# Performance work log

Hardware: AMD Instinct MI355X
Metric: run time of the kernel (lower is better)

Reference implementation:

```python
import jax, jax.numpy as jnp
import numpy as np

# Hard-coded model hyperparams (RuntimeParams)
B, L, H, NH, FF, DEPTH = 256, 256, 128, 8, 512, 4
PEAK, NCAT, CVOC, KMAX, NNUM, NDIM, TSLOT = 500000, 8, 50001, 8, 4, 32, 256
SCALE = (H // NH) ** -0.5


def _ln(x, g, b):
    m = x.mean(-1, keepdims=True)
    v = ((x - m) ** 2).mean(-1, keepdims=True)
    return (x - m) / jnp.sqrt(v + 1e-5) * g + b


def _block(x, mask, p):
    ln1_g, ln1_b, qw, qb, ow, ob, w1, b1, w2, b2, ln2_g, ln2_b = p
    b, n, c = x.shape
    src = _ln(x, ln1_g, ln1_b)
    qkv = (src @ qw + qb).reshape(b, n, 3, NH, c // NH).transpose(2, 0, 3, 1, 4)
    q, k, v = qkv[0], qkv[1], qkv[2]  # [b, nh, n, dh]
    dots = jnp.einsum('bhid,bhjd->bhij', q, k) * SCALE
    dots = jnp.where(mask[:, None, None, :], dots, -jnp.inf)
    attn = jax.nn.softmax(dots, axis=-1)
    out = jnp.einsum('bhij,bhjd->bhid', attn, v).transpose(0, 2, 1, 3).reshape(b, n, c)
    x = x + out @ ow + ob
    h = _ln(x, ln2_g, ln2_b)
    h = jax.nn.gelu(h @ w1 + b1, approximate=False) @ w2 + b2
    return x + h


def _encode(cat_vals, cat_lens, num_arr, cat_tables, num_W):
    # Vectorized form of the per-sample _encode_fields python loop:
    # per categorical field: mean of embeddings over the ragged value list
    # per numeric field: bias-free linear projection; then mean over all fields.
    emb = cat_tables[jnp.arange(NCAT)[None, :, None], cat_vals]  # [B,F,K,H]
    pos = (jnp.arange(KMAX)[None, None, :] < cat_lens[:, :, None]).astype(emb.dtype)
    fc = (emb * pos[..., None]).sum(2) / cat_lens[:, :, None].astype(emb.dtype)  # [B,F,H]
    fn = jnp.einsum('bfd,fdh->bfh', num_arr, num_W)  # [B,Fn,H]
    return (fc.sum(1) + fn.sum(1)) / (NCAT + NNUM)  # mean over all fields


def setup_inputs() -> dict:
    key = jax.random.key(0)
    ks = iter(jax.random.split(key, 40))
    nk = lambda: next(ks)
    d = {}
    d['item_seq'] = jax.random.randint(nk(), (B, L), 0, PEAK + 5)
    d['action_seq'] = jax.random.randint(nk(), (B, L), 0, 5)
    d['time_diff'] = jax.random.randint(nk(), (B, L), 0, TSLOT)
    seq_lens = jax.random.randint(nk(), (B,), L // 2, L + 1)
    d['mask'] = jnp.arange(L)[None, :] < seq_lens[:, None]
    for pre in ('u', 'i'):
        vals = jax.random.randint(nk(), (B, NCAT, KMAX), 1, CVOC)
        lens = jax.random.randint(nk(), (B, NCAT), 1, KMAX + 1)
        vals = jnp.where(jnp.arange(KMAX)[None, None, :] < lens[:, :, None], vals, 0)
        d[pre + '_cat_vals'] = vals
        d[pre + '_cat_lens'] = lens
        d[pre + '_num'] = jax.random.normal(nk(), (B, NNUM, NDIM), dtype=jnp.float32)
    s = 0.02
    d['item_table'] = (jax.random.normal(nk(), (PEAK + 5, H), dtype=jnp.float32) * s).at[0].set(0.0)
    d['act_table'] = jax.random.normal(nk(), (5, H), dtype=jnp.float32) * s
    d['time_table'] = jax.random.normal(nk(), (TSLOT, H), dtype=jnp.float32) * s
    d['cat_tables'] = (jax.random.normal(nk(), (NCAT, CVOC, H), dtype=jnp.float32) * s).at[:, 0, :].set(0.0)
    d['num_W'] = jax.random.normal(nk(), (NNUM, NDIM, H), dtype=jnp.float32) * s
    d['global_token'] = jax.random.normal(nk(), (1, 1, H), dtype=jnp.float32)
    d['ln1_g'] = jnp.ones((DEPTH, H)); d['ln1_b'] = jnp.zeros((DEPTH, H))
    d['qkv_w'] = jax.random.normal(nk(), (DEPTH, H, 3 * H), dtype=jnp.float32) * s
    d['qkv_b'] = jnp.zeros((DEPTH, 3 * H))
    d['out_w'] = jax.random.normal(nk(), (DEPTH, H, H), dtype=jnp.float32) * s
    d['out_b'] = jnp.zeros((DEPTH, H))
    d['mlp_w1'] = jax.random.normal(nk(), (DEPTH, H, FF), dtype=jnp.float32) * s
    d['mlp_b1'] = jnp.zeros((DEPTH, FF))
    d['mlp_w2'] = jax.random.normal(nk(), (DEPTH, FF, H), dtype=jnp.float32) * s
    d['mlp_b2'] = jnp.zeros((DEPTH, H))
    d['ln2_g'] = jnp.ones((DEPTH, H)); d['ln2_b'] = jnp.zeros((DEPTH, H))
    d['bott_w'] = jax.random.normal(nk(), (H, H), dtype=jnp.float32) * s
    d['bott_b'] = jnp.zeros((H,))
    d['cls_w'] = jax.random.normal(nk(), (H, 1), dtype=jnp.float32) * s
    d['cls_b'] = jnp.zeros((1,))
    return d


def reference(item_seq, action_seq, time_diff, mask, u_cat_vals, u_cat_lens, u_num,
              i_cat_vals, i_cat_lens, i_num, item_table, act_table, time_table,
              cat_tables, num_W, global_token, ln1_g, ln1_b, qkv_w, qkv_b,
              out_w, out_b, mlp_w1, mlp_b1, mlp_w2, mlp_b2, ln2_g, ln2_b,
              bott_w, bott_b, cls_w, cls_b):
    b = item_seq.shape[0]
    seq_feat = item_table[item_seq] + act_table[action_seq] + time_table[time_diff]  # [B,L,H]
    u = _encode(u_cat_vals, u_cat_lens, u_num, cat_tables, num_W)[:, None, :]
    i = _encode(i_cat_vals, i_cat_lens, i_num, cat_tables, num_W)[:, None, :]
    cls = jnp.broadcast_to(global_token, (b, 1, H))
    x = jnp.concatenate([cls, u, i, seq_feat], axis=1)  # [B, 3+L, H]
    fmask = jnp.concatenate([jnp.ones((b, 3), dtype=bool), mask], axis=1)
    for dd in range(DEPTH):
        p = (ln1_g[dd], ln1_b[dd], qkv_w[dd], qkv_b[dd], out_w[dd], out_b[dd],
             mlp_w1[dd], mlp_b1[dd], mlp_w2[dd], mlp_b2[dd], ln2_g[dd], ln2_b[dd])
        x = _block(x, fmask, p)
    latent = x[:, 0, :]
    logits = (jax.nn.relu(latent @ bott_w + bott_b) @ cls_w + cls_b)[:, 0]
    embed = latent / jnp.maximum(jnp.linalg.norm(latent, axis=-1, keepdims=True), 1e-12)
    return logits, embed
```

## Files before the change

### kernel.cpp

```cpp
#include <hip/hip_runtime.h>
#include <cstdio>

#define BATCH 256
#define SEQL 256
#define NPOS 259
#define TTOK (BATCH*NPOS)
#define HD 128
#define NHEAD 8
#define FF 512
#define DEPTH 4
#define CVOC 50001

typedef unsigned short u16;
typedef unsigned int u32;
typedef __bf16 bf16x8 __attribute__((ext_vector_type(8)));
typedef float f32x4 __attribute__((ext_vector_type(4)));
typedef float f32x16 __attribute__((ext_vector_type(16)));

typedef const __attribute__((address_space(1))) u32 gas_u32;
typedef __attribute__((address_space(3))) u32 las_u32;
#define GLOAD16(gptr, lptr) \
  __builtin_amdgcn_global_load_lds((gas_u32*)(gptr), (las_u32*)(lptr), 16, 0, 0)

#define QSCALE 0.36067376022224085f

__device__ __forceinline__ u16 f2bf(float f) {
  u32 i = __float_as_uint(f);
  u32 r = (i + 0x7FFFu + ((i >> 16) & 1u)) >> 16;
  return (u16)r;
}

__global__ void k_transpose_all(const float* __restrict__ qkv_w, const float* __restrict__ out_w,
                                const float* __restrict__ w1, const float* __restrict__ w2,
                                u16* __restrict__ wT) {
  int idx = blockIdx.x * 256 + threadIdx.x;
  const float* in; int K, N, local;
  if (idx < 196608)      { in = qkv_w; K = 128; N = 384; local = idx; }
  else if (idx < 262144) { in = out_w; K = 128; N = 128; local = idx - 196608; }
  else if (idx < 524288) { in = w1;    K = 128; N = 512; local = idx - 262144; }
  else if (idx < 786432) { in = w2;    K = 512; N = 128; local = idx - 524288; }
  else return;
  int k = local % K; int rem = local / K; int n = rem % N; int d = rem / N;
  wT[idx] = f2bf(in[(d * K + k) * N + n]);
}

__global__ __launch_bounds__(128)
void k_build(const int* __restrict__ item_seq, const int* __restrict__ act_seq,
             const int* __restrict__ tdiff,
             const int* __restrict__ ucv, const int* __restrict__ ucl, const float* __restrict__ unum,
             const int* __restrict__ icv, const int* __restrict__ icl, const float* __restrict__ inum,
             const float* __restrict__ item_t, const float* __restrict__ act_t,
             const float* __restrict__ time_t, const float* __restrict__ cat_t,
             const float* __restrict__ numW, const float* __restrict__ gtok,
             const float* __restrict__ g, const float* __restrict__ be,
             float* __restrict__ x, u16* __restrict__ src) {
  int pos = blockIdx.x, b = blockIdx.y, h = threadIdx.x;
  float v;
  if (pos == 0) {
    v = gtok[h];
  } else if (pos <= 2) {
    const int* cv = (pos == 1) ? ucv : icv;
    const int* cl = (pos == 1) ? ucl : icl;
    const float* nm = (pos == 1) ? unum : inum;
    float acc = 0.f;
    for (int f = 0; f < 8; ++f) {
      float s = 0.f;
      for (int k = 0; k < 8; ++k) {
        int idx = cv[(b * 8 + f) * 8 + k];
        s += cat_t[((size_t)f * CVOC + idx) * HD + h];
      }
      acc += s / (float)cl[b * 8 + f];
    }
    for (int f = 0; f < 4; ++f)
      for (int d = 0; d < 32; ++d)
        acc += nm[(b * 4 + f) * 32 + d] * numW[(f * 32 + d) * HD + h];
    v = acc * (1.f / 12.f);
  } else {
    int l = pos - 3;
    v = item_t[(size_t)item_seq[b * SEQL + l] * HD + h]
      + act_t[(size_t)act_seq[b * SEQL + l] * HD + h]
      + time_t[(size_t)tdiff[b * SEQL + l] * HD + h];
  }
  size_t t = (size_t)b * NPOS + pos;
  x[t * HD + h] = v;
  __shared__ float red[2][2];
  float s = v, s2 = v * v;
  #pragma unroll
  for (int o = 32; o; o >>= 1) { s += __shfl_xor(s, o); s2 += __shfl_xor(s2, o); }
  if ((h & 63) == 0) { red[h >> 6][0] = s; red[h >> 6][1] = s2; }
  __syncthreads();
  float S = red[0][0] + red[1][0], S2 = red[0][1] + red[1][1];
  float mean = S * (1.f / HD);
  float rstd = rsqrtf(S2 * (1.f / HD) - mean * mean + 1e-5f);
  src[t * HD + h] = f2bf((v - mean) * rstd * g[h] + be[h]);
}

template <int NCH, int ACT, bool QS>
__global__ __launch_bounds__(256)
void k_gemm_nres(const u16* __restrict__ X, const u16* __restrict__ WT,
                 const float* __restrict__ bias, u16* __restrict__ outp) {
  const int K = 128, N = NCH * 128;
  __shared__ __align__(16) u16 lA[4][128 * 32];
  __shared__ __align__(16) u16 lB[128 * 32];
  const int tid = threadIdx.x;
  const int wave = tid >> 6, lane = tid & 63;
  const int row0 = blockIdx.x * 128;
  const int wr = (wave >> 1) * 64, wc = (wave & 1) * 64;
  const int sr = lane >> 2;
  const int sc = ((lane & 3) ^ ((lane >> 3) & 3)) << 3;
  const int q = lane & 15;
  const int cg = lane >> 4;
  const int rdoff = ((cg ^ ((q >> 1) & 3)) << 3);
  #pragma unroll
  for (int s = 0; s < 8; ++s) {
    int kt = s & 3, rg = 2 * wave + (s >> 2);
    int r = rg * 16 + sr;
    GLOAD16(X + (size_t)(row0 + r) * K + kt * 32 + sc, &lA[kt][rg * 512]);
  }
  const u16* gB0 = WT + (size_t)(wave * 16 + sr) * K + sc;
  const u16* gB1 = WT + (size_t)(64 + wave * 16 + sr) * K + sc;
  u16* lB0 = &lB[wave * 512];
  u16* lB1 = &lB[2048 + wave * 512];
  for (int nc = 0; nc < NCH; ++nc) {
    const size_t nbase = (size_t)nc * 128 * K;
    f32x4 acc[4][4] = {};
    for (int k0 = 0; k0 < K; k0 += 32) {
      __syncthreads();
      GLOAD16(gB0 + nbase + k0, lB0);
      GLOAD16(gB1 + nbase + k0, lB1);
      __syncthreads();
      const int kt = k0 >> 5;
      bf16x8 af[4], bf[4];
      #pragma unroll
      for (int i = 0; i < 4; ++i)
        af[i] = *(const bf16x8*)&lA[kt][(wr + i * 16 + q) * 32 + rdoff];
      #pragma unroll
      for (int j = 0; j < 4; ++j)
        bf[j] = *(const bf16x8*)&lB[(wc + j * 16 + q) * 32 + rdoff];
      #pragma unroll
      for (int i = 0; i < 4; ++i)
        #pragma unroll
        for (int j = 0; j < 4; ++j)
          acc[i][j] = __builtin_amdgcn_mfma_f32_16x16x32_bf16(af[i], bf[j], acc[i][j], 0, 0, 0);
    }
    const int rg4 = cg * 4;
    const float scl = (QS && nc == 0) ? QSCALE : 1.f;
    #pragma unroll
    for (int i = 0; i < 4; ++i) {
      #pragma unroll
      for (int j = 0; j < 4; ++j) {
        int col = nc * 128 + wc + j * 16 + q;
        float bv = bias[col];
        #pragma unroll
        for (int jj = 0; jj < 4; ++jj) {
          int row = row0 + wr + i * 16 + rg4 + jj;
          float v = acc[i][j][jj] + bv;
          if (ACT == 1) v = 0.5f * v * (1.f + erff(v * 0.70710678118654752f));
          if (QS) v *= scl;
          outp[(size_t)row * N + col] = f2bf(v);
        }
      }
    }
  }
}

__global__ __launch_bounds__(256)
void k_gemm_ln(const u16* __restrict__ X, const u16* __restrict__ WT,
               const float* __restrict__ bias, float* __restrict__ xio,
               const float* __restrict__ g, const float* __restrict__ be,
               u16* __restrict__ srcout, int K) {
  __shared__ __align__(16) u16 lA[128 * 32];
  __shared__ __align__(16) u16 lB[128 * 32];
  __shared__ float part[128][2][2];
  const int tid = threadIdx.x;
  const int wave = tid >> 6, lane = tid & 63;
  const int row0 = blockIdx.x * 128;
  const int wr = (wave >> 1) * 64, wc = (wave & 1) * 64;
  const int whalf = wave & 1;
  const int sr = lane >> 2;
  const int sc = ((lane & 3) ^ ((lane >> 3) & 3)) << 3;
  const u16* gA0 = X  + (size_t)(row0 + wave * 16 + sr) * K + sc;
  const u16* gA1 = X  + (size_t)(row0 + 64 + wave * 16 + sr) * K + sc;
  const u16* gB0 = WT + (size_t)(wave * 16 + sr) * K + sc;
  const u16* gB1 = WT + (size_t)(64 + wave * 16 + sr) * K + sc;
  u16* lA0 = &lA[wave * 512];
  u16* lA1 = &lA[2048 + wave * 512];
  u16* lB0 = &lB[wave * 512];
  u16* lB1 = &lB[2048 + wave * 512];
  const int q = lane & 15;
  const int cg = lane >> 4;
  const int rdoff = ((cg ^ ((q >> 1) & 3)) << 3);
  f32x4 acc[4][4] = {};
  for (int k0 = 0; k0 < K; k0 += 32) {
    __syncthreads();
    GLOAD16(gA0 + k0, lA0);
    GLOAD16(gA1 + k0, lA1);
    GLOAD16(gB0 + k0, lB0);
    GLOAD16(gB1 + k0, lB1);
    __syncthreads();
    bf16x8 af[4], bf[4];
    #pragma unroll
    for (int i = 0; i < 4; ++i)
      af[i] = *(const bf16x8*)&lA[(wr + i * 16 + q) * 32 + rdoff];
    #pragma unroll
    for (int j = 0; j < 4; ++j)
      bf[j] = *(const bf16x8*)&lB[(wc + j * 16 + q) * 32 + rdoff];
    #pragma unroll
    for (int i = 0; i < 4; ++i)
      #pragma unroll
      for (int j = 0; j < 4; ++j)
        acc[i][j] = __builtin_amdgcn_mfma_f32_16x16x32_bf16(af[i], bf[j], acc[i][j], 0, 0, 0);
  }
  const int rg4 = cg * 4;
  float ps[4][4], ps2[4][4];
  #pragma unroll
  for (int i = 0; i < 4; ++i)
    #pragma unroll
    for (int jj = 0; jj < 4; ++jj) { ps[i][jj] = 0.f; ps2[i][jj] = 0.f; }
  #pragma unroll
  for (int i = 0; i < 4; ++i) {
    #pragma unroll
    for (int j = 0; j < 4; ++j) {
      int col = wc + j * 16 + q;
      float bv = bias[col];
      #pragma unroll
      for (int jj = 0; jj < 4; ++jj) {
        int row = row0 + wr + i * 16 + rg4 + jj;
        float xv = xio[(size_t)row * 128 + col] + acc[i][j][jj] + bv;
        acc[i][j][jj] = xv;
        ps[i][jj] += xv;
        ps2[i][jj] += xv * xv;
      }
    }
  }
  #pragma unroll
  for (int o = 1; o < 16; o <<= 1) {
    #pragma unroll
    for (int i = 0; i < 4; ++i)
      #pragma unroll
      for (int jj = 0; jj < 4; ++jj) {
        ps[i][jj]  += __shfl_xor(ps[i][jj], o);
        ps2[i][jj] += __shfl_xor(ps2[i][jj], o);
      }
  }
  if (q == 0) {
    #pragma unroll
    for (int i = 0; i < 4; ++i)
      #pragma unroll
      for (int jj = 0; jj < 4; ++jj) {
        int rl = wr + i * 16 + rg4 + jj;
        part[rl][whalf][0] = ps[i][jj];
        part[rl][whalf][1] = ps2[i][jj];
      }
  }
  __syncthreads();
  #pragma unroll
  for (int i = 0; i < 4; ++i) {
    #pragma unroll
    for (int jj = 0; jj < 4; ++jj) {
      int rl = wr + i * 16 + rg4 + jj;
      float S  = part[rl][0][0] + part[rl][1][0];
      float S2 = part[rl][0][1] + part[rl][1][1];
      float mean = S * (1.f / 128.f);
      float rstd = rsqrtf(S2 * (1.f / 128.f) - mean * mean + 1e-5f);
      int row = row0 + rl;
      #pragma unroll
      for (int j = 0; j < 4; ++j) {
        int col = wc + j * 16 + q;
        float xv = acc[i][j][jj];
        xio[(size_t)row * 128 + col] = xv;
        srcout[(size_t)row * 128 + col] = f2bf((xv - mean) * rstd * g[col] + be[col]);
      }
    }
  }
}

#define VSTR2 296
__global__ __launch_bounds__(576)
void k_attn(const u16* __restrict__ qkv, const int* __restrict__ mask,
            u16* __restrict__ out) {
  int h = blockIdx.x, b = blockIdx.y;
  __shared__ __align__(16) u16 Klin[9 * 512];
  __shared__ __align__(16) u16 Vt[16 * VSTR2];
  __shared__ int part[4];
  const int tid = threadIdx.x;
  if (tid < 256) {
    int mv = (mask[b * SEQL + tid] != 0) ? 1 : 0;
    #pragma unroll
    for (int o = 32; o; o >>= 1) mv += __shfl_xor(mv, o);
    if ((tid & 63) == 0) part[tid >> 6] = mv;
  }
  {
    int r = tid >> 1, h2 = tid & 1;
    uint4 val = make_uint4(0, 0, 0, 0);
    if (r < NPOS)
      val = *(const uint4*)&qkv[((size_t)(b * NPOS + r)) * 384 + h * 16 + 128 + h2 * 8];
    *(uint4*)&Klin[(r >> 5) * 512 + h2 * 256 + (r & 31) * 8] = val;
  }
  if (tid < 288) {
    int r = tid;
    u16 tmp[16];
    if (r < NPOS) {
      const u16* vp = &qkv[((size_t)(b * NPOS + r)) * 384 + h * 16 + 256];
      *(uint4*)&tmp[0] = *(const uint4*)&vp[0];
      *(uint4*)&tmp[8] = *(const uint4*)&vp[8];
    } else {
      #pragma unroll
      for (int d = 0; d < 16; ++d) tmp[d] = 0;
    }
    #pragma unroll
    for (int d = 0; d < 16; ++d) Vt[d * VSTR2 + r] = tmp[d];
  }
  __syncthreads();
  const int nvalid = part[0] + part[1] + part[2] + part[3] + 3;
  const int ktiles = (nvalid + 31) >> 5;
  const int wave = tid >> 6, lane = tid & 63;
  const int q5 = lane & 31, hi = lane >> 5;
  const f32x16 zf = {};
  const int qt = wave;
  int qrow = qt * 32 + q5;
  int qr = (qrow < NPOS) ? qrow : (NPOS - 1);
  bf16x8 qf = *(const bf16x8*)&qkv[((size_t)(b * NPOS + qr)) * 384 + h * 16 + hi * 8];
  float m = -1e30f, l = 0.f;
  f32x16 acc = {};
  for (int kt = 0; kt < ktiles; ++kt) {
    bf16x8 kf = *(const bf16x8*)&Klin[kt * 512 + lane * 8];
    __builtin_amdgcn_s_setprio(1);
    f32x16 s4 = __builtin_amdgcn_mfma_f32_32x32x16_bf16(kf, qf, zf, 0, 0, 0);
    __builtin_amdgcn_s_setprio(0);
    float p[16];
    float tmax = -1e30f;
    #pragma unroll
    for (int r = 0; r < 16; ++r) {
      int kr = kt * 32 + (r & 3) + 8 * (r >> 2) + 4 * hi;
      float v = (kr < nvalid) ? s4[r] : -1e30f;
      p[r] = v;
      tmax = fmaxf(tmax, v);
    }
    tmax = fmaxf(tmax, __shfl_xor(tmax, 32));
    float mnew = fmaxf(m, tmax);
    float fac = exp2f(m - mnew);
    float tsum = 0.f;
    #pragma unroll
    for (int r = 0; r < 16; ++r) { p[r] = exp2f(p[r] - mnew); tsum += p[r]; }
    tsum += __shfl_xor(tsum, 32);
    l = l * fac + tsum;
    m = mnew;
    #pragma unroll
    for (int r = 0; r < 8; ++r) acc[r] *= fac;
    u32 w[8], xw[8];
    #pragma unroll
    for (int i = 0; i < 8; ++i)
      asm("v_cvt_pk_bf16_f32 %0, %1, %2" : "=v"(w[i]) : "v"(p[2 * i]), "v"(p[2 * i + 1]));
    #pragma unroll
    for (int i = 0; i < 8; ++i) xw[i] = (u32)__shfl_xor((int)w[i], 32);
    union { u32 u[4]; bf16x8 v; } f1, f2;
    if (hi) {
      f1.u[0] = xw[2]; f1.u[1] = xw[3]; f1.u[2] = w[2]; f1.u[3] = w[3];
      f2.u[0] = xw[6]; f2.u[1] = xw[7]; f2.u[2] = w[6]; f2.u[3] = w[7];
    } else {
      f1.u[0] = w[0]; f1.u[1] = w[1]; f1.u[2] = xw[0]; f1.u[3] = xw[1];
      f2.u[0] = w[4]; f2.u[1] = w[5]; f2.u[2] = xw[4]; f2.u[3] = xw[5];
    }
    bf16x8 vf0 = {}, vf1 = {};
    if (q5 < 16) {
      vf0 = *(const bf16x8*)&Vt[q5 * VSTR2 + kt * 32 + hi * 8];
      vf1 = *(const bf16x8*)&Vt[q5 * VSTR2 + kt * 32 + 16 + hi * 8];
    }
    __builtin_amdgcn_s_setprio(1);
    acc = __builtin_amdgcn_mfma_f32_32x32x16_bf16(vf0, f1.v, acc, 0, 0, 0);
    acc = __builtin_amdgcn_mfma_f32_32x32x16_bf16(vf1, f2.v, acc, 0, 0, 0);
    __builtin_amdgcn_s_setprio(0);
  }
  if (qrow < NPOS) {
    float linv = 1.f / l;
    u16* op = &out[((size_t)(b * NPOS + qrow)) * HD + h * 16];
    u32 w0 = (u32)f2bf(acc[0] * linv) | ((u32)f2bf(acc[1] * linv) << 16);
    u32 w1 = (u32)f2bf(acc[2] * linv) | ((u32)f2bf(acc[3] * linv) << 16);
    u32 w2 = (u32)f2bf(acc[4] * linv) | ((u32)f2bf(acc[5] * linv) << 16);
    u32 w3 = (u32)f2bf(acc[6] * linv) | ((u32)f2bf(acc[7] * linv) << 16);
    *(uint2*)&op[4 * hi] = make_uint2(w0, w1);
    *(uint2*)&op[8 + 4 * hi] = make_uint2(w2, w3);
  }
}

__global__ __launch_bounds__(128)
void k_head(const float* __restrict__ x, const float* __restrict__ bw,
            const float* __restrict__ bb, const float* __restrict__ cw,
            const float* __restrict__ cb, float* __restrict__ dout) {
  int b = blockIdx.x, n = threadIdx.x;
  __shared__ float lat[HD];
  __shared__ float redp[2], redss[2];
  float lv = x[((size_t)b * NPOS) * HD + n];
  lat[n] = lv;
  __syncthreads();
  float t = 0.f;
  for (int k = 0; k < HD; ++k) t += lat[k] * bw[k * HD + n];
  t += bb[n];
  t = fmaxf(t, 0.f);
  float p = t * cw[n];
  float ss = lv * lv;
  #pragma unroll
  for (int o = 32; o; o >>= 1) { p += __shfl_xor(p, o); ss += __shfl_xor(ss, o); }
  if ((n & 63) == 0) { redp[n >> 6] = p; redss[n >> 6] = ss; }
  __syncthreads();
  float psum = redp[0] + redp[1];
  float ssum = redss[0] + redss[1];
  if (n == 0) dout[b] = psum + cb[0];
  float nrm = fmaxf(sqrtf(ssum), 1e-12f);
  dout[256 + (size_t)b * HD + n] = lv / nrm;
}

extern "C" void kernel_launch(void* const* d_in, const int* in_sizes, int n_in,
                              void* d_out, int out_size, void* d_ws, size_t ws_size,
                              hipStream_t stream) {
  const int* item_seq = (const int*)d_in[0];
  const int* action_seq = (const int*)d_in[1];
  const int* time_diff = (const int*)d_in[2];
  const int* mask = (const int*)d_in[3];
  const int* u_cv = (const int*)d_in[4];
  const int* u_cl = (const int*)d_in[5];
  const float* u_num = (const float*)d_in[6];
  const int* i_cv = (const int*)d_in[7];
  const int* i_cl = (const int*)d_in[8];
  const float* i_num = (const float*)d_in[9];
  const float* item_t = (const float*)d_in[10];
  const float* act_t = (const float*)d_in[11];
  const float* time_t = (const float*)d_in[12];
  const float* cat_t = (const float*)d_in[13];
  const float* num_W = (const float*)d_in[14];
  const float* gtok = (const float*)d_in[15];
  const float* ln1_g = (const float*)d_in[16];
  const float* ln1_b = (const float*)d_in[17];
  const float* qkv_w = (const float*)d_in[18];
  const float* qkv_b = (const float*)d_in[19];
  const float* out_w = (const float*)d_in[20];
  const float* out_b = (const float*)d_in[21];
  const float* w1 = (const float*)d_in[22];
  const float* b1 = (const float*)d_in[23];
  const float* w2 = (const float*)d_in[24];
  const float* b2 = (const float*)d_in[25];
  const float* ln2_g = (const float*)d_in[26];
  const float* ln2_b = (const float*)d_in[27];
  const float* bott_w = (const float*)d_in[28];
  const float* bott_b = (const float*)d_in[29];
  const float* cls_w = (const float*)d_in[30];
  const float* cls_b = (const float*)d_in[31];

  const size_t off_x   = 0;
  const size_t off_src = 33947648;
  const size_t off_big = 50921472;
  const size_t off_wT  = 118816768;
  const size_t need    = 120389632;
  if (ws_size < need) {
    fprintf(stderr, "kernel_launch: ws_size %zu < needed %zu\n", ws_size, need);
    return;
  }
  char* ws = (char*)d_ws;
  float* x   = (float*)(ws + off_x);
  u16* src   = (u16*)(ws + off_src);
  u16* big   = (u16*)(ws + off_big);
  u16* wT    = (u16*)(ws + off_wT);
  u16* qkvT  = wT;
  u16* outT  = wT + 196608;
  u16* w1T   = wT + 262144;
  u16* w2T   = wT + 524288;

  k_transpose_all<<<3072, 256, 0, stream>>>(qkv_w, out_w, w1, w2, wT);

  k_build<<<dim3(NPOS, BATCH), 128, 0, stream>>>(
      item_seq, action_seq, time_diff, u_cv, u_cl, u_num, i_cv, i_cl, i_num,
      item_t, act_t, time_t, cat_t, num_W, gtok, ln1_g, ln1_b, x, src);

  const int rt = TTOK / 128;
  for (int dd = 0; dd < DEPTH; ++dd) {
    k_gemm_nres<3, 0, true><<<rt, 256, 0, stream>>>(
        src, qkvT + dd * 49152, qkv_b + dd * 384, big);
    k_attn<<<dim3(NHEAD, BATCH), 576, 0, stream>>>(big, mask, src);
    k_gemm_ln<<<dim3(rt, 1), 256, 0, stream>>>(
        src, outT + dd * 16384, out_b + dd * HD, x,
        ln2_g + dd * HD, ln2_b + dd * HD, src, 128);
    k_gemm_nres<4, 1, false><<<rt, 256, 0, stream>>>(
        src, w1T + dd * 65536, b1 + dd * FF, big);
    const float* ng = (dd < 3) ? (ln1_g + (dd + 1) * HD) : (ln1_g + dd * HD);
    const float* nb = (dd < 3) ? (ln1_b + (dd + 1) * HD) : (ln1_b + dd * HD);
    k_gemm_ln<<<dim3(rt, 1), 256, 0, stream>>>(
        big, w2T + dd * 65536, b2 + dd * HD, x, ng, nb, src, 512);
  }

  k_head<<<BATCH, 128, 0, stream>>>(x, bott_w, bott_b, cls_w, cls_b, (float*)d_out);
}
```

Measured before the change: 784.8 us.

## Fuse residual-LayerNorm GEMMs with following QKV and MLP-up GEMMs via LDS-resident activations

Merges each residual+LayerNorm GEMM with the GEMM that consumes its output. The normalized 128-wide tile is written into shared memory in the swizzled layout and reused directly as the A operand for the next GEMM: MLP up-projection with GELU, or the next layer's QKV projection with Q scaling. This removes the bf16 round-trip of the LN output through global memory and two kernel launches per layer. In exchange each block does more serial work, uses more shared memory, and the workspace grows to hold separate QKV and hidden buffers. The last layer uses a plain residual GEMM instead.

```diff
diff --git a/kernel.cpp b/kernel.cpp
--- a/kernel.cpp
+++ b/kernel.cpp
@@ -164,19 +164,176 @@
   }
 }
 
+template <int K1, int NCH2, int ACT2, bool QS2>
 __global__ __launch_bounds__(256)
-void k_gemm_ln(const u16* __restrict__ X, const u16* __restrict__ WT,
-               const float* __restrict__ bias, float* __restrict__ xio,
-               const float* __restrict__ g, const float* __restrict__ be,
-               u16* __restrict__ srcout, int K) {
-  __shared__ __align__(16) u16 lA[128 * 32];
-  __shared__ __align__(16) u16 lB[128 * 32];
+void k_fused(const u16* __restrict__ X, const u16* __restrict__ WT1,
+             const float* __restrict__ bias1, float* __restrict__ xio,
+             const float* __restrict__ g, const float* __restrict__ be,
+             const u16* __restrict__ WT2, const float* __restrict__ bias2,
+             u16* __restrict__ out2) {
+  __shared__ __align__(16) u16 sA[4][128 * 32];
+  __shared__ __align__(16) u16 sB[128 * 32];
   __shared__ float part[128][2][2];
   const int tid = threadIdx.x;
   const int wave = tid >> 6, lane = tid & 63;
   const int row0 = blockIdx.x * 128;
   const int wr = (wave >> 1) * 64, wc = (wave & 1) * 64;
   const int whalf = wave & 1;
+  const int sr = lane >> 2;
+  const int sc = ((lane & 3) ^ ((lane >> 3) & 3)) << 3;
+  const int q = lane & 15;
+  const int cg = lane >> 4;
+  const int rdoff = ((cg ^ ((q >> 1) & 3)) << 3);
+  const int rg4 = cg * 4;
+  {
+    const u16* gA0 = X + (size_t)(row0 + wave * 16 + sr) * K1 + sc;
+    const u16* gA1 = X + (size_t)(row0 + 64 + wave * 16 + sr) * K1 + sc;
+    const u16* gB0 = WT1 + (size_t)(wave * 16 + sr) * K1 + sc;
+    const u16* gB1 = WT1 + (size_t)(64 + wave * 16 + sr) * K1 + sc;
+    u16* lA0 = &sA[0][wave * 512];
+    u16* lA1 = &sA[0][2048 + wave * 512];
+    u16* lB0 = &sB[wave * 512];
+    u16* lB1 = &sB[2048 + wave * 512];
+    f32x4 acc[4][4] = {};
+    for (int k0 = 0; k0 < K1; k0 += 32) {
+      __syncthreads();
+      GLOAD16(gA0 + k0, lA0);
+      GLOAD16(gA1 + k0, lA1);
+      GLOAD16(gB0 + k0, lB0);
+      GLOAD16(gB1 + k0, lB1);
+      __syncthreads();
+      bf16x8 af[4], bf[4];
+      #pragma unroll
+      for (int i = 0; i < 4; ++i)
+        af[i] = *(const bf16x8*)&sA[0][(wr + i * 16 + q) * 32 + rdoff];
+      #pragma unroll
+      for (int j = 0; j < 4; ++j)
+        bf[j] = *(const bf16x8*)&sB[(wc + j * 16 + q) * 32 + rdoff];
+      #pragma unroll
+      for (int i = 0; i < 4; ++i)
+        #pragma unroll
+        for (int j = 0; j < 4; ++j)
+          acc[i][j] = __builtin_amdgcn_mfma_f32_16x16x32_bf16(af[i], bf[j], acc[i][j], 0, 0, 0);
+    }
+    float ps[4][4], ps2[4][4];
+    #pragma unroll
+    for (int i = 0; i < 4; ++i)
+      #pragma unroll
+      for (int jj = 0; jj < 4; ++jj) { ps[i][jj] = 0.f; ps2[i][jj] = 0.f; }
+    #pragma unroll
+    for (int i = 0; i < 4; ++i) {
+      #pragma unroll
+      for (int j = 0; j < 4; ++j) {
+        int col = wc + j * 16 + q;
+        float bv = bias1[col];
+        #pragma unroll
+        for (int jj = 0; jj < 4; ++jj) {
+          int row = row0 + wr + i * 16 + rg4 + jj;
+          float xv = xio[(size_t)row * 128 + col] + acc[i][j][jj] + bv;
+          acc[i][j][jj] = xv;
+          ps[i][jj] += xv;
+          ps2[i][jj] += xv * xv;
+        }
+      }
+    }
+    #pragma unroll
+    for (int o = 1; o < 16; o <<= 1) {
+      #pragma unroll
+      for (int i = 0; i < 4; ++i)
+        #pragma unroll
+        for (int jj = 0; jj < 4; ++jj) {
+          ps[i][jj]  += __shfl_xor(ps[i][jj], o);
+          ps2[i][jj] += __shfl_xor(ps2[i][jj], o);
+        }
+    }
+    if (q == 0) {
+      #pragma unroll
+      for (int i = 0; i < 4; ++i)
+        #pragma unroll
+        for (int jj = 0; jj < 4; ++jj) {
+          int rl = wr + i * 16 + rg4 + jj;
+          part[rl][whalf][0] = ps[i][jj];
+          part[rl][whalf][1] = ps2[i][jj];
+        }
+    }
+    __syncthreads();
+    #pragma unroll
+    for (int i = 0; i < 4; ++i) {
+      #pragma unroll
+      for (int jj = 0; jj < 4; ++jj) {
+        int rl = wr + i * 16 + rg4 + jj;
+        float S  = part[rl][0][0] + part[rl][1][0];
+        float S2 = part[rl][0][1] + part[rl][1][1];
+        float mean = S * (1.f / 128.f);
+        float rstd = rsqrtf(S2 * (1.f / 128.f) - mean * mean + 1e-5f);
+        int row = row0 + rl;
+        const int rsel = ((rl >> 1) & 3);
+        #pragma unroll
+        for (int j = 0; j < 4; ++j) {
+          int col = wc + j * 16 + q;
+          float xv = acc[i][j][jj];
+          xio[(size_t)row * 128 + col] = xv;
+          u16 lnv = f2bf((xv - mean) * rstd * g[col] + be[col]);
+          sA[col >> 5][rl * 32 + ((((col >> 3) & 3) ^ rsel) << 3) + (col & 7)] = lnv;
+        }
+      }
+    }
+  }
+  const u16* gB20 = WT2 + (size_t)(wave * 16 + sr) * 128 + sc;
+  const u16* gB21 = WT2 + (size_t)(64 + wave * 16 + sr) * 128 + sc;
+  u16* lB0 = &sB[wave * 512];
+  u16* lB1 = &sB[2048 + wave * 512];
+  for (int nc = 0; nc < NCH2; ++nc) {
+    const size_t nbase = (size_t)nc * 128 * 128;
+    f32x4 acc[4][4] = {};
+    for (int k0 = 0; k0 < 128; k0 += 32) {
+      __syncthreads();
+      GLOAD16(gB20 + nbase + k0, lB0);
+      GLOAD16(gB21 + nbase + k0, lB1);
+      __syncthreads();
+      const int kt = k0 >> 5;
+      bf16x8 af[4], bf[4];
+      #pragma unroll
+      for (int i = 0; i < 4; ++i)
+        af[i] = *(const bf16x8*)&sA[kt][(wr + i * 16 + q) * 32 + rdoff];
+      #pragma unroll
+      for (int j = 0; j < 4; ++j)
+        bf[j] = *(const bf16x8*)&sB[(wc + j * 16 + q) * 32 + rdoff];
+      #pragma unroll
+      for (int i = 0; i < 4; ++i)
+        #pragma unroll
+        for (int j = 0; j < 4; ++j)
+          acc[i][j] = __builtin_amdgcn_mfma_f32_16x16x32_bf16(af[i], bf[j], acc[i][j], 0, 0, 0);
+    }
+    const float scl = (QS2 && nc == 0) ? QSCALE : 1.f;
+    #pragma unroll
+    for (int i = 0; i < 4; ++i) {
+      #pragma unroll
+      for (int j = 0; j < 4; ++j) {
+        int col = nc * 128 + wc + j * 16 + q;
+        float bv = bias2[col];
+        #pragma unroll
+        for (int jj = 0; jj < 4; ++jj) {
+          int row = row0 + wr + i * 16 + rg4 + jj;
+          float v = acc[i][j][jj] + bv;
+          if (ACT2 == 1) v = 0.5f * v * (1.f + erff(v * 0.70710678118654752f));
+          if (QS2) v *= scl;
+          out2[(size_t)row * (NCH2 * 128) + col] = f2bf(v);
+        }
+      }
+    }
+  }
+}
+
+__global__ __launch_bounds__(256)
+void k_gemm_res(const u16* __restrict__ X, const u16* __restrict__ WT,
+                const float* __restrict__ bias, float* __restrict__ xio, int K) {
+  __shared__ __align__(16) u16 lA[128 * 32];
+  __shared__ __align__(16) u16 lB[128 * 32];
+  const int tid = threadIdx.x;
+  const int wave = tid >> 6, lane = tid & 63;
+  const int row0 = blockIdx.x * 128;
+  const int wr = (wave >> 1) * 64, wc = (wave & 1) * 64;
   const int sr = lane >> 2;
   const int sc = ((lane & 3) ^ ((lane >> 3) & 3)) << 3;
   const u16* gA0 = X  + (size_t)(row0 + wave * 16 + sr) * K + sc;
@@ -212,11 +369,6 @@
         acc[i][j] = __builtin_amdgcn_mfma_f32_16x16x32_bf16(af[i], bf[j], acc[i][j], 0, 0, 0);
   }
   const int rg4 = cg * 4;
-  float ps[4][4], ps2[4][4];
-  #pragma unroll
-  for (int i = 0; i < 4; ++i)
-    #pragma unroll
-    for (int jj = 0; jj < 4; ++jj) { ps[i][jj] = 0.f; ps2[i][jj] = 0.f; }
   #pragma unroll
   for (int i = 0; i < 4; ++i) {
     #pragma unroll
@@ -226,50 +378,7 @@
       #pragma unroll
       for (int jj = 0; jj < 4; ++jj) {
         int row = row0 + wr + i * 16 + rg4 + jj;
-        float xv = xio[(size_t)row * 128 + col] + acc[i][j][jj] + bv;
-        acc[i][j][jj] = xv;
-        ps[i][jj] += xv;
-        ps2[i][jj] += xv * xv;
-      }
-    }
-  }
-  #pragma unroll
-  for (int o = 1; o < 16; o <<= 1) {
-    #pragma unroll
-    for (int i = 0; i < 4; ++i)
-      #pragma unroll
-      for (int jj = 0; jj < 4; ++jj) {
-        ps[i][jj]  += __shfl_xor(ps[i][jj], o);
-        ps2[i][jj] += __shfl_xor(ps2[i][jj], o);
-      }
-  }
-  if (q == 0) {
-    #pragma unroll
-    for (int i = 0; i < 4; ++i)
-      #pragma unroll
-      for (int jj = 0; jj < 4; ++jj) {
-        int rl = wr + i * 16 + rg4 + jj;
-        part[rl][whalf][0] = ps[i][jj];
-        part[rl][whalf][1] = ps2[i][jj];
-      }
-  }
-  __syncthreads();
-  #pragma unroll
-  for (int i = 0; i < 4; ++i) {
-    #pragma unroll
-    for (int jj = 0; jj < 4; ++jj) {
-      int rl = wr + i * 16 + rg4 + jj;
-      float S  = part[rl][0][0] + part[rl][1][0];
-      float S2 = part[rl][0][1] + part[rl][1][1];
-      float mean = S * (1.f / 128.f);
-      float rstd = rsqrtf(S2 * (1.f / 128.f) - mean * mean + 1e-5f);
-      int row = row0 + rl;
-      #pragma unroll
-      for (int j = 0; j < 4; ++j) {
-        int col = wc + j * 16 + q;
-        float xv = acc[i][j][jj];
-        xio[(size_t)row * 128 + col] = xv;
-        srcout[(size_t)row * 128 + col] = f2bf((xv - mean) * rstd * g[col] + be[col]);
+        xio[(size_t)row * 128 + col] += acc[i][j][jj] + bv;
       }
     }
   }
@@ -447,24 +556,26 @@
   const float* cls_w = (const float*)d_in[30];
   const float* cls_b = (const float*)d_in[31];
 
-  const size_t off_x   = 0;
-  const size_t off_src = 33947648;
-  const size_t off_big = 50921472;
-  const size_t off_wT  = 118816768;
-  const size_t need    = 120389632;
+  const size_t off_x    = 0;
+  const size_t off_src  = 33947648;
+  const size_t off_qkv  = 50921472;
+  const size_t off_h1   = 101842944;
+  const size_t off_wT   = 169738240;
+  const size_t need     = 171311104;
   if (ws_size < need) {
     fprintf(stderr, "kernel_launch: ws_size %zu < needed %zu\n", ws_size, need);
     return;
   }
   char* ws = (char*)d_ws;
-  float* x   = (float*)(ws + off_x);
-  u16* src   = (u16*)(ws + off_src);
-  u16* big   = (u16*)(ws + off_big);
-  u16* wT    = (u16*)(ws + off_wT);
-  u16* qkvT  = wT;
-  u16* outT  = wT + 196608;
-  u16* w1T   = wT + 262144;
-  u16* w2T   = wT + 524288;
+  float* x    = (float*)(ws + off_x);
+  u16* src    = (u16*)(ws + off_src);
+  u16* qkvbuf = (u16*)(ws + off_qkv);
+  u16* h1buf  = (u16*)(ws + off_h1);
+  u16* wT     = (u16*)(ws + off_wT);
+  u16* qkvT   = wT;
+  u16* outT   = wT + 196608;
+  u16* w1T    = wT + 262144;
+  u16* w2T    = wT + 524288;
 
   k_transpose_all<<<3072, 256, 0, stream>>>(qkv_w, out_w, w1, w2, wT);
 
@@ -473,19 +584,22 @@
       item_t, act_t, time_t, cat_t, num_W, gtok, ln1_g, ln1_b, x, src);
 
   const int rt = TTOK / 128;
+  k_gemm_nres<3, 0, true><<<rt, 256, 0, stream>>>(src, qkvT, qkv_b, qkvbuf);
+
   for (int dd = 0; dd < DEPTH; ++dd) {
-    k_gemm_nres<3, 0, true><<<rt, 256, 0, stream>>>(
-        src, qkvT + dd * 49152, qkv_b + dd * 384, big);
-    k_attn<<<dim3(NHEAD, BATCH), 576, 0, stream>>>(big, mask, src);
-    k_gemm_ln<<<dim3(rt, 1), 256, 0, stream>>>(
+    k_attn<<<dim3(NHEAD, BATCH), 576, 0, stream>>>(qkvbuf, mask, src);
+    k_fused<128, 4, 1, false><<<rt, 256, 0, stream>>>(
         src, outT + dd * 16384, out_b + dd * HD, x,
-        ln2_g + dd * HD, ln2_b + dd * HD, src, 128);
-    k_gemm_nres<4, 1, false><<<rt, 256, 0, stream>>>(
-        src, w1T + dd * 65536, b1 + dd * FF, big);
-    const float* ng = (dd < 3) ? (ln1_g + (dd + 1) * HD) : (ln1_g + dd * HD);
-    const float* nb = (dd < 3) ? (ln1_b + (dd + 1) * HD) : (ln1_b + dd * HD);
-    k_gemm_ln<<<dim3(rt, 1), 256, 0, stream>>>(
-        big, w2T + dd * 65536, b2 + dd * HD, x, ng, nb, src, 512);
+        ln2_g + dd * HD, ln2_b + dd * HD,
+        w1T + dd * 65536, b1 + dd * FF, h1buf);
+    if (dd < 3) {
+      k_fused<512, 3, 0, true><<<rt, 256, 0, stream>>>(
+          h1buf, w2T + dd * 65536, b2 + dd * HD, x,
+          ln1_g + (dd + 1) * HD, ln1_b + (dd + 1) * HD,
+          qkvT + (dd + 1) * 49152, qkv_b + (dd + 1) * 384, qkvbuf);
+    } else {
+      k_gemm_res<<<rt, 256, 0, stream>>>(h1buf, w2T + dd * 65536, b2 + dd * HD, x, 512);
+    }
   }
 
   k_head<<<BATCH, 128, 0, stream>>>(x, bott_w, bott_b, cls_w, cls_b, (float*)d_out);
```

Measured after the change: 1.018 ms. +29.7%, slower.
